# Optimization experiments

Hardware: AMD Instinct MI355X
Metric: run time of the kernel (lower is better)

The kernel has to match this reference:

```python
import jax, jax.numpy as jnp
import numpy as np

IN_DIM = 512
OUT_DIM = 512
LEAKY_SLOPE = 0.01
LN_EPS = 1e-5


def setup_inputs() -> dict:
    key = jax.random.key(0)
    ks = jax.random.split(key, 5)
    x = jax.random.normal(ks[0], (8, 2048, IN_DIM), dtype=jnp.float32)
    ln_gamma = jnp.ones((IN_DIM,), dtype=jnp.float32)
    ln_beta = jnp.zeros((IN_DIM,), dtype=jnp.float32)
    # torch Linear weight is [out, in]; store transposed [in, out] for x @ W
    W_qkv = jax.random.normal(ks[1], (IN_DIM, 3 * IN_DIM), dtype=jnp.float32) * (IN_DIM ** -0.5)
    W_fc = jax.random.normal(ks[2], (IN_DIM, OUT_DIM), dtype=jnp.float32) * (IN_DIM ** -0.5)
    b_fc = jax.random.normal(ks[3], (OUT_DIM,), dtype=jnp.float32) * 0.01
    return {"x": x, "ln_gamma": ln_gamma, "ln_beta": ln_beta,
            "W_qkv": W_qkv, "W_fc": W_fc, "b_fc": b_fc}


def reference(x, ln_gamma, ln_beta, W_qkv, W_fc, b_fc):
    scale = IN_DIM ** -0.5
    # LayerNorm over last dim
    mu = jnp.mean(x, axis=-1, keepdims=True)
    var = jnp.var(x, axis=-1, keepdims=True)
    xn = (x - mu) * jax.lax.rsqrt(var + LN_EPS) * ln_gamma + ln_beta
    # fused QKV projection, chunk into thirds
    qkv = xn @ W_qkv  # [B,S,3D]
    q, k, v = jnp.split(qkv, 3, axis=-1)
    # naive full attention: softmax((q k^T) * scale) v
    w = jnp.einsum('bsd,btd->bst', q, k) * scale
    attn = jax.nn.softmax(w, axis=-1)
    o = jnp.einsum('bst,btd->bsd', attn, v)
    # FC + LeakyReLU
    y = o @ W_fc + b_fc
    return jnp.where(y >= 0, y, LEAKY_SLOPE * y)
```

## Files before the change

### kernel.cpp

```cpp
#include <hip/hip_runtime.h>
#include <hip/hip_bf16.h>


typedef _Float16 f16;
typedef f16 f16x8 __attribute__((ext_vector_type(8)));
typedef float f32x4 __attribute__((ext_vector_type(4)));
typedef unsigned short u16;
typedef u16 u16x8 __attribute__((ext_vector_type(8)));

#define BK 32

enum { EPI_F16 = 0, EPI_BIAS_LEAKY = 1, EPI_EXPL = 2, EPI_NORM = 3 };

__device__ __forceinline__ void stage16(const void* g, void* l) {
    __builtin_amdgcn_global_load_lds((const __attribute__((address_space(1))) void*)g,
                                     (__attribute__((address_space(3))) void*)l,
                                     16, 0, 0);
}

__device__ __forceinline__ int rhash(int r) { return (r & 3) ^ ((r >> 2) & 3); }

struct GemmP {
    const f16 *ah, *ah2;
    const f16 *bh;
    float* cf;
    f16 *chi, *chi2;
    const float* bias;
    float* lsum;
    long long aStride, bStride, cStride, lStride;
    int lda, ldb, ldc, K, zSplit;
    float scale;
};

template <int BMt, int BNt, int EPI>
__global__ __launch_bounds__(256, 2) void gemm_k(GemmP p) {
    constexpr int NISSA = BMt / 64;
    constexpr int NISSB = BNt / 64;
    constexpr int FRm = BMt / 32;
    constexpr int FRn = BNt / 32;

    __shared__ __align__(16) f16 sA[BMt * BK];
    __shared__ __align__(16) f16 sB[BNt * BK];

    const int tid  = threadIdx.x;
    const int w    = tid >> 6;
    const int lane = tid & 63;

    const int gx = gridDim.x;
    const int nwg = gx * gridDim.y * gridDim.z;
    const int flat = (blockIdx.z * gridDim.y + blockIdx.y) * gx + blockIdx.x;
    const int nf = (flat & 7) * (nwg >> 3) + (flat >> 3);
    const int bx = nf % gx;
    const int by = (nf / gx) % gridDim.y;
    const long long zb = nf / (gx * gridDim.y);

    const int m0 = by * BMt;
    const int n0 = bx * BNt;

    const f16* ah = (zb < p.zSplit) ? p.ah + zb * p.aStride
                                    : p.ah2 + (zb - p.zSplit) * p.aStride;
    const f16* bh = p.bh + zb * p.bStride;

    const int srow = tid >> 2;
    const int scol = (((tid & 3) ^ rhash(tid >> 2)) * 8);
    size_t aOff[NISSA], bOff[NISSB];
#pragma unroll
    for (int i = 0; i < NISSA; ++i) aOff[i] = (size_t)(m0 + i * 64 + srow) * p.lda + scol;
#pragma unroll
    for (int i = 0; i < NISSB; ++i) bOff[i] = (size_t)(n0 + i * 64 + srow) * p.ldb + scol;
    const int ldsW = w * 512;

    const int fr = lane & 15;
    const int fg = lane >> 4;
    const int wr = (w >> 1) * (BMt / 2);
    const int wc = (w & 1) * (BNt / 2);
    const int aBase = (wr + fr) * BK + ((fg ^ rhash(fr)) * 8);
    const int bBase = (wc + fr) * BK + ((fg ^ rhash(fr)) * 8);

    const f32x4 fzero = {0.f, 0.f, 0.f, 0.f};
    f32x4 acc[FRm][FRn];
#pragma unroll
    for (int i = 0; i < FRm; ++i)
#pragma unroll
        for (int j = 0; j < FRn; ++j) acc[i][j] = fzero;

    for (int kk = 0; kk < p.K; kk += BK) {
#pragma unroll
        for (int i = 0; i < NISSA; ++i) stage16(ah + aOff[i] + kk, sA + i * 2048 + ldsW);
#pragma unroll
        for (int i = 0; i < NISSB; ++i) stage16(bh + bOff[i] + kk, sB + i * 2048 + ldsW);
        __syncthreads();

        f16x8 fa[FRm], fb[FRn];
#pragma unroll
        for (int i = 0; i < FRm; ++i) fa[i] = *(const f16x8*)(sA + aBase + i * 16 * BK);
#pragma unroll
        for (int j = 0; j < FRn; ++j) fb[j] = *(const f16x8*)(sB + bBase + j * 16 * BK);
#pragma unroll
        for (int i = 0; i < FRm; ++i)
#pragma unroll
            for (int j = 0; j < FRn; ++j)
                acc[i][j] = __builtin_amdgcn_mfma_f32_16x16x32_f16(fa[i], fb[j], acc[i][j], 0, 0, 0);
        __syncthreads();
    }

    const int erow = m0 + wr + fg * 4;
    const int ecol = n0 + wc + fr;

    if constexpr (EPI == EPI_EXPL) {
        f16* cb = (zb < p.zSplit) ? p.chi + zb * p.cStride
                                  : p.chi2 + (zb - p.zSplit) * p.cStride;
        float rs[FRm][4];
#pragma unroll
        for (int i = 0; i < FRm; ++i)
#pragma unroll
            for (int r = 0; r < 4; ++r) rs[i][r] = 0.f;
#pragma unroll
        for (int i = 0; i < FRm; ++i)
#pragma unroll
            for (int j = 0; j < FRn; ++j)
#pragma unroll
                for (int r = 0; r < 4; ++r) {
                    const float pv = __expf(acc[i][j][r] * p.scale);
                    const f16 h = (f16)pv;
                    cb[(size_t)(erow + i * 16 + r) * p.ldc + (ecol + j * 16)] = h;
                    rs[i][r] += (float)h;
                }
#pragma unroll
        for (int i = 0; i < FRm; ++i)
#pragma unroll
            for (int r = 0; r < 4; ++r) {
                float s = rs[i][r];
                s += __shfl_xor(s, 1, 64); s += __shfl_xor(s, 2, 64);
                s += __shfl_xor(s, 4, 64); s += __shfl_xor(s, 8, 64);
                if (fr == 0) atomicAdd(p.lsum + zb * p.lStride + (erow + i * 16 + r), s);
            }
    } else if constexpr (EPI == EPI_NORM) {
#pragma unroll
        for (int i = 0; i < FRm; ++i)
#pragma unroll
            for (int r = 0; r < 4; ++r) {
                const float inv = 1.0f / p.lsum[zb * p.lStride + (erow + i * 16 + r)];
#pragma unroll
                for (int j = 0; j < FRn; ++j) {
                    const size_t idx = (size_t)(erow + i * 16 + r) * p.ldc + (ecol + j * 16);
                    (p.chi + zb * p.cStride)[idx] = (f16)(acc[i][j][r] * inv);
                }
            }
    } else {
#pragma unroll
        for (int i = 0; i < FRm; ++i)
#pragma unroll
            for (int j = 0; j < FRn; ++j)
#pragma unroll
                for (int r = 0; r < 4; ++r) {
                    const size_t idx = (size_t)(erow + i * 16 + r) * p.ldc + (ecol + j * 16);
                    const float v = acc[i][j][r];
                    if constexpr (EPI == EPI_F16) {
                        (p.chi + zb * p.cStride)[idx] = (f16)v;
                    } else {
                        float y = v + p.bias[ecol + j * 16];
                        (p.cf + zb * p.cStride)[idx] = (y >= 0.f) ? y : 0.01f * y;
                    }
                }
    }
}

__global__ __launch_bounds__(256) void ln_k(const float* x, const float* gw, const float* bw,
                                            f16* ah) {
    const int row  = blockIdx.x * 4 + (threadIdx.x >> 6);
    const int lane = threadIdx.x & 63;
    const float* xr = x + (size_t)row * 512;
    float4 u = *(const float4*)(xr + lane * 8);
    float4 v = *(const float4*)(xr + lane * 8 + 4);
    float s = u.x + u.y + u.z + u.w + v.x + v.y + v.z + v.w;
#pragma unroll
    for (int off = 32; off; off >>= 1) s += __shfl_xor(s, off, 64);
    const float mu = s * (1.f / 512.f);
    float d[8] = {u.x - mu, u.y - mu, u.z - mu, u.w - mu,
                  v.x - mu, v.y - mu, v.z - mu, v.w - mu};
    float q = 0.f;
#pragma unroll
    for (int j = 0; j < 8; ++j) q += d[j] * d[j];
#pragma unroll
    for (int off = 32; off; off >>= 1) q += __shfl_xor(q, off, 64);
    const float rstd = 1.0f / sqrtf(q * (1.f / 512.f) + 1e-5f);
    float4 g1 = *(const float4*)(gw + lane * 8);
    float4 g2 = *(const float4*)(gw + lane * 8 + 4);
    float4 b1 = *(const float4*)(bw + lane * 8);
    float4 b2 = *(const float4*)(bw + lane * 8 + 4);
    float gg[8] = {g1.x, g1.y, g1.z, g1.w, g2.x, g2.y, g2.z, g2.w};
    float bb[8] = {b1.x, b1.y, b1.z, b1.w, b2.x, b2.y, b2.z, b2.w};
    f16x8 hv;
#pragma unroll
    for (int j = 0; j < 8; ++j) hv[j] = (f16)(d[j] * rstd * gg[j] + bb[j]);
    *(f16x8*)(ah + (size_t)row * 512 + lane * 8) = hv;
}

__global__ __launch_bounds__(256) void wsplit_k(const float* W, int N, f16* wh) {
    const int i = blockIdx.x * 256 + threadIdx.x;
    if (i >= N * 512) return;
    const int n = i >> 9, k = i & 511;
    wh[i] = (f16)W[(size_t)k * N + n];
}

__global__ __launch_bounds__(256) void transpose_v_k(const f16* qh, f16* vth) {
    __shared__ u16 th[64][65];
    const int b  = blockIdx.z;
    const int s0 = blockIdx.x * 64;
    const int d0 = blockIdx.y * 64;
    const int tid = threadIdx.x;
#pragma unroll
    for (int pp = 0; pp < 2; ++pp) {
        const int idx = tid * 8 + pp * 2048;
        const int sl = idx >> 6, dl = idx & 63;
        const size_t src = ((size_t)(b * 2048 + s0 + sl)) * 1536 + 1024 + d0 + dl;
        u16x8 hv = *(const u16x8*)(qh + src);
#pragma unroll
        for (int j = 0; j < 8; ++j) th[sl][dl + j] = hv[j];
    }
    __syncthreads();
#pragma unroll
    for (int pp = 0; pp < 2; ++pp) {
        const int idx = tid * 8 + pp * 2048;
        const int dl = idx >> 6, sl = idx & 63;
        u16x8 hv;
#pragma unroll
        for (int j = 0; j < 8; ++j) hv[j] = th[sl + j][dl];
        const size_t dst = ((size_t)(b * 512 + d0 + dl)) * 2048 + s0 + sl;
        *(u16x8*)(vth + dst) = hv;
    }
}

extern "C" void kernel_launch(void* const* d_in, const int* in_sizes, int n_in,
                              void* d_out, int out_size, void* d_ws, size_t ws_size,
                              hipStream_t stream) {
    const float* x     = (const float*)d_in[0];
    const float* gamma = (const float*)d_in[1];
    const float* beta  = (const float*)d_in[2];
    const float* Wqkv  = (const float*)d_in[3];
    const float* Wfc   = (const float*)d_in[4];
    const float* bfc   = (const float*)d_in[5];
    float* out = (float*)d_out;

    char* w = (char*)d_ws;
    f16* wqt    = (f16*)w; w += (size_t)1536 * 512 * 2;
    f16* wft    = (f16*)w; w += (size_t)512 * 512 * 2;
    float* l    = (float*)w; w += (size_t)8 * 2048 * 4;
    f16* a_hi   = (f16*)w; w += (size_t)16384 * 512 * 2;
    f16* qkv    = (f16*)w; w += (size_t)16384 * 1536 * 2;

    f16* vt   = a_hi;
    f16* o_hi = qkv + 1024;
    f16* P0 = (f16*)d_in[0];
    f16* P1 = (f16*)d_out;
    const long long PSTR = (long long)2048 * 2048;
    const long long QKVSTR = (long long)2048 * 1536;

    hipMemsetAsync(l, 0, (size_t)8 * 2048 * 4, stream);
    ln_k<<<4096, 256, 0, stream>>>(x, gamma, beta, a_hi);
    wsplit_k<<<(1536 * 512) / 256, 256, 0, stream>>>(Wqkv, 1536, wqt);
    wsplit_k<<<(512 * 512) / 256, 256, 0, stream>>>(Wfc, 512, wft);

    GemmP pq{};
    pq.ah = a_hi; pq.ah2 = a_hi; pq.bh = wqt;
    pq.aStride = 0; pq.bStride = 0; pq.cStride = 0; pq.zSplit = 1 << 30;
    pq.lda = 512; pq.ldb = 512; pq.ldc = 1536; pq.K = 512;
    pq.chi = qkv;
    gemm_k<128, 128, EPI_F16><<<dim3(12, 128, 1), 256, 0, stream>>>(pq);

    transpose_v_k<<<dim3(32, 8, 8), 256, 0, stream>>>(qkv, vt);

    GemmP ps{};
    ps.ah = qkv; ps.ah2 = qkv + 4 * QKVSTR;
    ps.bh = qkv + 512;
    ps.aStride = QKVSTR; ps.bStride = QKVSTR;
    ps.cStride = PSTR; ps.lStride = 2048; ps.zSplit = 4;
    ps.lda = 1536; ps.ldb = 1536; ps.ldc = 2048; ps.K = 512;
    ps.chi = P0; ps.chi2 = P1;
    ps.lsum = l;
    ps.scale = 0.044194173824159216f;
    gemm_k<128, 128, EPI_EXPL><<<dim3(16, 16, 8), 256, 0, stream>>>(ps);

    GemmP pp{};
    pp.ah = P0; pp.ah2 = P1;
    pp.bh = vt;
    pp.aStride = PSTR; pp.bStride = (long long)512 * 2048;
    pp.cStride = QKVSTR; pp.lStride = 2048; pp.zSplit = 4;
    pp.lda = 2048; pp.ldb = 2048; pp.ldc = 1536; pp.K = 2048;
    pp.chi = o_hi;
    pp.lsum = l;
    gemm_k<128, 128, EPI_NORM><<<dim3(4, 16, 8), 256, 0, stream>>>(pp);

    GemmP pf{};
    pf.ah = o_hi; pf.ah2 = o_hi; pf.bh = wft;
    pf.aStride = 0; pf.bStride = 0; pf.cStride = 0; pf.zSplit = 1 << 30;
    pf.lda = 1536; pf.ldb = 512; pf.ldc = 512; pf.K = 512;
    pf.cf = out; pf.bias = bfc;
    gemm_k<128, 128, EPI_BIAS_LEAKY><<<dim3(4, 128, 1), 256, 0, stream>>>(pf);
}
```

Baseline: 281.5 us.

## Double-buffer LDS tiles in GEMM to overlap global loads with MFMA

```diff
diff --git a/kernel.cpp b/kernel.cpp
--- a/kernel.cpp
+++ b/kernel.cpp
@@ -33,14 +33,14 @@
 };
 
 template <int BMt, int BNt, int EPI>
-__global__ __launch_bounds__(256, 2) void gemm_k(GemmP p) {
+__global__ __launch_bounds__(256, 4) void gemm_k(GemmP p) {
     constexpr int NISSA = BMt / 64;
     constexpr int NISSB = BNt / 64;
     constexpr int FRm = BMt / 32;
     constexpr int FRn = BNt / 32;
 
-    __shared__ __align__(16) f16 sA[BMt * BK];
-    __shared__ __align__(16) f16 sB[BNt * BK];
+    __shared__ __align__(16) f16 sA[2][BMt * BK];
+    __shared__ __align__(16) f16 sB[2][BNt * BK];
 
     const int tid  = threadIdx.x;
     const int w    = tid >> 6;
@@ -84,24 +84,39 @@
 #pragma unroll
         for (int j = 0; j < FRn; ++j) acc[i][j] = fzero;
 
-    for (int kk = 0; kk < p.K; kk += BK) {
-#pragma unroll
-        for (int i = 0; i < NISSA; ++i) stage16(ah + aOff[i] + kk, sA + i * 2048 + ldsW);
-#pragma unroll
-        for (int i = 0; i < NISSB; ++i) stage16(bh + bOff[i] + kk, sB + i * 2048 + ldsW);
-        __syncthreads();
-
+#pragma unroll
+    for (int i = 0; i < NISSA; ++i) stage16(ah + aOff[i], &sA[0][i * 2048 + ldsW]);
+#pragma unroll
+    for (int i = 0; i < NISSB; ++i) stage16(bh + bOff[i], &sB[0][i * 2048 + ldsW]);
+    asm volatile("s_waitcnt vmcnt(0)" ::: "memory");
+    __builtin_amdgcn_s_barrier();
+
+    const int nt = p.K / BK;
+    int cur = 0;
+    for (int t = 0; t < nt; ++t) {
+        if (t + 1 < nt) {
+            const int kk = (t + 1) * BK;
+#pragma unroll
+            for (int i = 0; i < NISSA; ++i)
+                stage16(ah + aOff[i] + kk, &sA[cur ^ 1][i * 2048 + ldsW]);
+#pragma unroll
+            for (int i = 0; i < NISSB; ++i)
+                stage16(bh + bOff[i] + kk, &sB[cur ^ 1][i * 2048 + ldsW]);
+        }
         f16x8 fa[FRm], fb[FRn];
 #pragma unroll
-        for (int i = 0; i < FRm; ++i) fa[i] = *(const f16x8*)(sA + aBase + i * 16 * BK);
-#pragma unroll
-        for (int j = 0; j < FRn; ++j) fb[j] = *(const f16x8*)(sB + bBase + j * 16 * BK);
+        for (int i = 0; i < FRm; ++i) fa[i] = *(const f16x8*)(&sA[cur][aBase + i * 16 * BK]);
+#pragma unroll
+        for (int j = 0; j < FRn; ++j) fb[j] = *(const f16x8*)(&sB[cur][bBase + j * 16 * BK]);
 #pragma unroll
         for (int i = 0; i < FRm; ++i)
 #pragma unroll
             for (int j = 0; j < FRn; ++j)
                 acc[i][j] = __builtin_amdgcn_mfma_f32_16x16x32_f16(fa[i], fb[j], acc[i][j], 0, 0, 0);
-        __syncthreads();
+        __builtin_amdgcn_sched_barrier(0);
+        asm volatile("s_waitcnt vmcnt(0)" ::: "memory");
+        __builtin_amdgcn_s_barrier();
+        cur ^= 1;
     }
 
     const int erow = m0 + wr + fg * 4;
```

Result: no change. 286.7 us (+1.8%).

## Stage GEMM epilogue through shared memory for coalesced vector stores

Applied to the files above, without the earlier changes.

```diff
diff --git a/kernel.cpp b/kernel.cpp
--- a/kernel.cpp
+++ b/kernel.cpp
@@ -33,14 +33,18 @@
 };
 
 template <int BMt, int BNt, int EPI>
-__global__ __launch_bounds__(256, 2) void gemm_k(GemmP p) {
+__global__ __launch_bounds__(256, 4) void gemm_k(GemmP p) {
     constexpr int NISSA = BMt / 64;
     constexpr int NISSB = BNt / 64;
     constexpr int FRm = BMt / 32;
     constexpr int FRn = BNt / 32;
-
-    __shared__ __align__(16) f16 sA[BMt * BK];
-    __shared__ __align__(16) f16 sB[BNt * BK];
+    constexpr int EROW = 130;
+    constexpr int LOOPB = (BMt + BNt) * BK * 2;
+    constexpr int EPIB  = 64 * EROW * 4;
+    __shared__ __align__(16) char pool[(LOOPB > EPIB) ? LOOPB : EPIB];
+    f16* sA  = (f16*)pool;
+    f16* sB  = (f16*)(pool + BMt * BK * 2);
+    float* sE = (float*)pool;
 
     const int tid  = threadIdx.x;
     const int w    = tid >> 6;
@@ -105,64 +109,102 @@
     }
 
     const int erow = m0 + wr + fg * 4;
-    const int ecol = n0 + wc + fr;
-
-    if constexpr (EPI == EPI_EXPL) {
-        f16* cb = (zb < p.zSplit) ? p.chi + zb * p.cStride
-                                  : p.chi2 + (zb - p.zSplit) * p.cStride;
-        float rs[FRm][4];
+    const int half = (wr != 0);
+
+    f16* cb = nullptr;
+    if constexpr (EPI == EPI_EXPL)
+        cb = (zb < p.zSplit) ? p.chi + zb * p.cStride
+                             : p.chi2 + (zb - p.zSplit) * p.cStride;
+    else if constexpr (EPI != EPI_BIAS_LEAKY)
+        cb = p.chi + zb * p.cStride;
+
+    float inv[FRm][4];
+    if constexpr (EPI == EPI_NORM) {
 #pragma unroll
         for (int i = 0; i < FRm; ++i)
 #pragma unroll
-            for (int r = 0; r < 4; ++r) rs[i][r] = 0.f;
-#pragma unroll
-        for (int i = 0; i < FRm; ++i)
-#pragma unroll
-            for (int j = 0; j < FRn; ++j)
-#pragma unroll
-                for (int r = 0; r < 4; ++r) {
-                    const float pv = __expf(acc[i][j][r] * p.scale);
-                    const f16 h = (f16)pv;
-                    cb[(size_t)(erow + i * 16 + r) * p.ldc + (ecol + j * 16)] = h;
-                    rs[i][r] += (float)h;
+            for (int r = 0; r < 4; ++r)
+                inv[i][r] = 1.0f / p.lsum[zb * p.lStride + (erow + i * 16 + r)];
+    }
+
+#pragma unroll
+    for (int h = 0; h < 2; ++h) {
+        if (half == h) {
+            float rs[FRm][4];
+            if constexpr (EPI == EPI_EXPL) {
+#pragma unroll
+                for (int i = 0; i < FRm; ++i)
+#pragma unroll
+                    for (int r = 0; r < 4; ++r) rs[i][r] = 0.f;
+            }
+#pragma unroll
+            for (int i = 0; i < FRm; ++i)
+#pragma unroll
+                for (int j = 0; j < FRn; ++j)
+#pragma unroll
+                    for (int r = 0; r < 4; ++r) {
+                        const int rowl = fg * 4 + i * 16 + r;
+                        const int col  = wc + fr + j * 16;
+                        const float v = acc[i][j][r];
+                        float sv;
+                        if constexpr (EPI == EPI_EXPL) {
+                            const float pv = exp2f(v * p.scale);
+                            sv = (float)(f16)pv;
+                            rs[i][r] += sv;
+                        } else if constexpr (EPI == EPI_NORM) {
+                            sv = v * inv[i][r];
+                        } else if constexpr (EPI == EPI_BIAS_LEAKY) {
+                            const float y = v + p.bias[n0 + col];
+                            sv = (y >= 0.f) ? y : 0.01f * y;
+                        } else {
+                            sv = v;
+                        }
+                        sE[rowl * EROW + col] = sv;
+                    }
+            if constexpr (EPI == EPI_EXPL) {
+#pragma unroll
+                for (int i = 0; i < FRm; ++i)
+#pragma unroll
+                    for (int r = 0; r < 4; ++r) {
+                        float s = rs[i][r];
+                        s += __shfl_xor(s, 1, 64); s += __shfl_xor(s, 2, 64);
+                        s += __shfl_xor(s, 4, 64); s += __shfl_xor(s, 8, 64);
+                        if (fr == 0)
+                            atomicAdd(p.lsum + zb * p.lStride + (erow + i * 16 + r), s);
+                    }
+            }
+        }
+        __syncthreads();
+        {
+            const int rowl  = tid >> 2;
+            const int grow  = m0 + h * 64 + rowl;
+            const int cbase = (tid & 3) * 32;
+            const float* se = sE + rowl * EROW + cbase;
+            if constexpr (EPI == EPI_BIAS_LEAKY) {
+                float* co = p.cf + zb * p.cStride + (size_t)grow * p.ldc + n0 + cbase;
+#pragma unroll
+                for (int k = 0; k < 8; ++k) {
+                    float2 a = *(const float2*)(se + k * 4);
+                    float2 b = *(const float2*)(se + k * 4 + 2);
+                    float4 f4 = {a.x, a.y, b.x, b.y};
+                    *(float4*)(co + k * 4) = f4;
                 }
-#pragma unroll
-        for (int i = 0; i < FRm; ++i)
-#pragma unroll
-            for (int r = 0; r < 4; ++r) {
-                float s = rs[i][r];
-                s += __shfl_xor(s, 1, 64); s += __shfl_xor(s, 2, 64);
-                s += __shfl_xor(s, 4, 64); s += __shfl_xor(s, 8, 64);
-                if (fr == 0) atomicAdd(p.lsum + zb * p.lStride + (erow + i * 16 + r), s);
-            }
-    } else if constexpr (EPI == EPI_NORM) {
-#pragma unroll
-        for (int i = 0; i < FRm; ++i)
-#pragma unroll
-            for (int r = 0; r < 4; ++r) {
-                const float inv = 1.0f / p.lsum[zb * p.lStride + (erow + i * 16 + r)];
-#pragma unroll
-                for (int j = 0; j < FRn; ++j) {
-                    const size_t idx = (size_t)(erow + i * 16 + r) * p.ldc + (ecol + j * 16);
-                    (p.chi + zb * p.cStride)[idx] = (f16)(acc[i][j][r] * inv);
+            } else {
+                f16* co = cb + (size_t)grow * p.ldc + n0 + cbase;
+#pragma unroll
+                for (int k = 0; k < 4; ++k) {
+                    float2 a = *(const float2*)(se + k * 8);
+                    float2 b = *(const float2*)(se + k * 8 + 2);
+                    float2 c = *(const float2*)(se + k * 8 + 4);
+                    float2 d = *(const float2*)(se + k * 8 + 6);
+                    f16x8 hv;
+                    hv[0] = (f16)a.x; hv[1] = (f16)a.y; hv[2] = (f16)b.x; hv[3] = (f16)b.y;
+                    hv[4] = (f16)c.x; hv[5] = (f16)c.y; hv[6] = (f16)d.x; hv[7] = (f16)d.y;
+                    *(f16x8*)(co + k * 8) = hv;
                 }
             }
-    } else {
-#pragma unroll
-        for (int i = 0; i < FRm; ++i)
-#pragma unroll
-            for (int j = 0; j < FRn; ++j)
-#pragma unroll
-                for (int r = 0; r < 4; ++r) {
-                    const size_t idx = (size_t)(erow + i * 16 + r) * p.ldc + (ecol + j * 16);
-                    const float v = acc[i][j][r];
-                    if constexpr (EPI == EPI_F16) {
-                        (p.chi + zb * p.cStride)[idx] = (f16)v;
-                    } else {
-                        float y = v + p.bias[ecol + j * 16];
-                        (p.cf + zb * p.cStride)[idx] = (y >= 0.f) ? y : 0.01f * y;
-                    }
-                }
+        }
+        __syncthreads();
     }
 }
 
@@ -279,7 +321,7 @@
     ps.lda = 1536; ps.ldb = 1536; ps.ldc = 2048; ps.K = 512;
     ps.chi = P0; ps.chi2 = P1;
     ps.lsum = l;
-    ps.scale = 0.044194173824159216f;
+    ps.scale = 0.06376353745687238f;
     gemm_k<128, 128, EPI_EXPL><<<dim3(16, 16, 8), 256, 0, stream>>>(ps);
 
     GemmP pp{};
```

After: 304.1 us. +8.0%, slower.
